# Performance work log

Hardware: AMD Instinct MI355X
Metric: run time of the kernel (lower is better)

The kernel has to match this reference:

```python
import jax, jax.numpy as jnp
import numpy as np

N_NODES = 50000
N_EDGES = 800000
F = 64
R = 32


def setup_inputs() -> dict:
    key = jax.random.key(0)
    ks = jax.random.split(key, 12)
    s = jax.random.normal(ks[0], (N_NODES, F), dtype=jnp.float32)
    v = jax.random.normal(ks[1], (N_NODES, 3, F), dtype=jnp.float32)
    radial_embeddings = jax.random.normal(ks[2], (N_EDGES, R), dtype=jnp.float32)
    f_cut = jax.random.uniform(ks[3], (N_EDGES,), dtype=jnp.float32)
    unit_vectors = jax.random.normal(ks[4], (N_EDGES, 3), dtype=jnp.float32)
    edge_index = jax.random.randint(ks[5], (2, N_EDGES), 0, N_NODES, dtype=jnp.int64 if jax.config.jax_enable_x64 else jnp.int32)
    # mlp_phi: Linear(F,F) -> SiLU -> Linear(F, 3F); linear_W: Linear(R, 3F)
    W1 = jax.random.normal(ks[6], (F, F), dtype=jnp.float32) / np.sqrt(F)
    b1 = jnp.zeros((F,), dtype=jnp.float32)
    W2 = jax.random.normal(ks[7], (F, 3 * F), dtype=jnp.float32) / np.sqrt(F)
    b2 = jnp.zeros((3 * F,), dtype=jnp.float32)
    Wr = jax.random.normal(ks[8], (R, 3 * F), dtype=jnp.float32) / np.sqrt(R)
    br = jnp.zeros((3 * F,), dtype=jnp.float32)
    return {"s": s, "v": v, "radial_embeddings": radial_embeddings, "f_cut": f_cut,
            "unit_vectors": unit_vectors, "edge_index": edge_index,
            "W1": W1, "b1": b1, "W2": W2, "b2": b2, "Wr": Wr, "br": br}


def reference(s, v, radial_embeddings, f_cut, unit_vectors, edge_index, W1, b1, W2, b2, Wr, br):
    idx_i, idx_j = edge_index[0], edge_index[1]
    n_nodes = s.shape[0]
    nf = s.shape[-1]
    # per-node MLP: Linear -> SiLU -> Linear to 3F channels
    phi = jax.nn.silu(s @ W1 + b1) @ W2 + b2            # [N, 3F]
    # radial filter weighted by cutoff
    W = (radial_embeddings @ Wr + br) * f_cut[:, None]   # [E, 3F]
    x = phi[idx_j] * W                                   # [E, 3F]  (gather + multiply)
    x_s, x_vv, x_vs = x[:, :nf], x[:, nf:2 * nf], x[:, 2 * nf:]
    ds = jax.ops.segment_sum(x_s, idx_i, num_segments=n_nodes)          # [N, F]
    x_v = v[idx_j] * x_vv[:, None, :] + x_vs[:, None, :] * unit_vectors[:, :, None]  # [E, 3, F]
    dv = jax.ops.segment_sum(x_v, idx_i, num_segments=n_nodes)          # [N, 3, F]
    return s + ds, v + dv
```

## Files before the change

kernel.cpp:

```cpp
#include <hip/hip_runtime.h>
#include <math.h>

#define N_NODES 50000
#define N_EDGES 800000
#define F 64
#define R 32
#define C3F 192
#define CAP 48
#define MLP_BLOCKS ((N_NODES + 31) / 32)
#define FILL_BLOCKS ((N_EDGES + 255) / 256)

#define REP32(X) X(0) X(1) X(2) X(3) X(4) X(5) X(6) X(7) \
                 X(8) X(9) X(10) X(11) X(12) X(13) X(14) X(15) \
                 X(16) X(17) X(18) X(19) X(20) X(21) X(22) X(23) \
                 X(24) X(25) X(26) X(27) X(28) X(29) X(30) X(31)

__global__ __launch_bounds__(256) void mlp_fill_kernel(
    const float* __restrict__ s, const float* __restrict__ W1,
    const float* __restrict__ b1, const float* __restrict__ W2,
    const float* __restrict__ b2, float* __restrict__ phi,
    const int* __restrict__ eidx, int* __restrict__ counts,
    int2* __restrict__ bucket)
{
    __shared__ float hid_s[32][68];

    if (blockIdx.x >= MLP_BLOCKS) {
        int e = (blockIdx.x - MLP_BLOCKS) * 256 + threadIdx.x;
        if (e < N_EDGES) {
            int i = eidx[e];
            int j = eidx[N_EDGES + e];
            int pos = atomicAdd(&counts[i], 1);
            if (pos < CAP) bucket[(size_t)i * CAP + pos] = make_int2(e, j);
        }
        return;
    }

    int n = threadIdx.x >> 3;
    int seg = threadIdx.x & 7;
    int node = blockIdx.x * 32 + n;
    bool live = node < N_NODES;

    if (live) {
        float sv[F];
        const float4* srow = (const float4*)(s + (size_t)node * F);
#pragma unroll
        for (int q = 0; q < F / 4; q++) {
            float4 t = srow[q];
            sv[4*q+0] = t.x; sv[4*q+1] = t.y; sv[4*q+2] = t.z; sv[4*q+3] = t.w;
        }
        float acc[8];
#pragma unroll
        for (int q = 0; q < 8; q++) acc[q] = b1[seg * 8 + q];
#pragma unroll
        for (int k = 0; k < F; k++) {
            float sk = sv[k];
            const float4* w = (const float4*)(W1 + (size_t)k * F + seg * 8);
            float4 w0 = w[0], w1 = w[1];
            acc[0] += sk * w0.x; acc[1] += sk * w0.y;
            acc[2] += sk * w0.z; acc[3] += sk * w0.w;
            acc[4] += sk * w1.x; acc[5] += sk * w1.y;
            acc[6] += sk * w1.z; acc[7] += sk * w1.w;
        }
#pragma unroll
        for (int q = 0; q < 8; q++) {
            float a = acc[q];
            hid_s[n][seg * 8 + q] = a / (1.f + __expf(-a));
        }
    }
    __syncthreads();

    if (!live) return;

    float hv[F];
#pragma unroll
    for (int q = 0; q < F; q++) hv[q] = hid_s[n][q];

    float acc[24];
#pragma unroll
    for (int q = 0; q < 24; q++) acc[q] = b2[seg * 24 + q];
#pragma unroll
    for (int k = 0; k < F; k++) {
        float hk = hv[k];
        const float4* w = (const float4*)(W2 + (size_t)k * C3F + seg * 24);
#pragma unroll
        for (int q4 = 0; q4 < 6; q4++) {
            float4 wv = w[q4];
            acc[q4*4+0] += hk * wv.x;
            acc[q4*4+1] += hk * wv.y;
            acc[q4*4+2] += hk * wv.z;
            acc[q4*4+3] += hk * wv.w;
        }
    }
    float4* o = (float4*)(phi + (size_t)node * C3F + seg * 24);
#pragma unroll
    for (int q4 = 0; q4 < 6; q4++)
        o[q4] = make_float4(acc[q4*4+0], acc[q4*4+1], acc[q4*4+2], acc[q4*4+3]);
}

__global__ __launch_bounds__(256, 3) void gather_kernel(
    const float* __restrict__ s, const float* __restrict__ v,
    const float* __restrict__ phi, const float* __restrict__ radial,
    const float* __restrict__ f_cut, const float* __restrict__ unit_vec,
    const float* __restrict__ Wr, const float* __restrict__ br,
    const int* __restrict__ counts, const int2* __restrict__ bucket,
    float* __restrict__ out_s, float* __restrict__ out_v)
{
    int lane = threadIdx.x & 63;
    int node = __builtin_amdgcn_readfirstlane(
        (int)blockIdx.x * 4 + (int)(threadIdx.x >> 6));
    if (node >= N_NODES) return;

#define DECL_WR(r) float wrs##r, wrv##r, wrq##r;
    REP32(DECL_WR)
#undef DECL_WR
#define LOAD_WR(r) { const float* w_ = Wr + (r) * C3F; \
                     wrs##r = w_[lane]; wrv##r = w_[64 + lane]; \
                     wrq##r = w_[128 + lane]; }
    REP32(LOAD_WR)
#undef LOAD_WR

    float b_s = br[lane], b_vv = br[64 + lane], b_vs = br[128 + lane];

    float acc_s = 0.f, acc_v0 = 0.f, acc_v1 = 0.f, acc_v2 = 0.f;

    int cnt = __builtin_amdgcn_readfirstlane(counts[node]);
    cnt = cnt < CAP ? cnt : CAP;
    const int2* row = bucket + (size_t)node * CAP;

    if (cnt > 0) {
        int2 ej0 = row[0];
        int e = __builtin_amdgcn_readfirstlane(ej0.x);
        int j = __builtin_amdgcn_readfirstlane(ej0.y);
        const float* pj = phi + (size_t)j * C3F;
        const float* vj = v + (size_t)j * C3F;
        float ps = pj[lane], pvv = pj[64 + lane], pvs = pj[128 + lane];
        float va = vj[lane], vb = vj[64 + lane], vc = vj[128 + lane];

        for (int k = 0; k < cnt; k++) {
            float fc = f_cut[e];
            float u0 = unit_vec[e * 3 + 0];
            float u1 = unit_vec[e * 3 + 1];
            float u2 = unit_vec[e * 3 + 2];
            const float* rp = radial + (size_t)e * R;

            int e_n = e, j_n = j;
            if (k + 1 < cnt) {
                int2 ejn = row[k + 1];
                e_n = __builtin_amdgcn_readfirstlane(ejn.x);
                j_n = __builtin_amdgcn_readfirstlane(ejn.y);
            }
            const float* pn = phi + (size_t)j_n * C3F;
            const float* vn = v + (size_t)j_n * C3F;
            float nps = pn[lane], npvv = pn[64 + lane], npvs = pn[128 + lane];
            float nva = vn[lane], nvb = vn[64 + lane], nvc = vn[128 + lane];

            float ws = b_s, wvv = b_vv, wvs = b_vs;
#define FMA_WR(r) { float rr = rp[r]; ws += rr * wrs##r; \
                    wvv += rr * wrv##r; wvs += rr * wrq##r; }
            REP32(FMA_WR)
#undef FMA_WR

            float xs  = ps  * ws  * fc;
            float xvv = pvv * wvv * fc;
            float xvs = pvs * wvs * fc;
            acc_s  += xs;
            acc_v0 += va * xvv + xvs * u0;
            acc_v1 += vb * xvv + xvs * u1;
            acc_v2 += vc * xvv + xvs * u2;

            e = e_n; j = j_n;
            ps = nps; pvv = npvv; pvs = npvs;
            va = nva; vb = nvb; vc = nvc;
        }
    }

    out_s[(size_t)node * F + lane] = s[(size_t)node * F + lane] + acc_s;
    const float* vi = v + (size_t)node * C3F;
    float* ovi = out_v + (size_t)node * C3F;
    ovi[lane]       = vi[lane]       + acc_v0;
    ovi[64 + lane]  = vi[64 + lane]  + acc_v1;
    ovi[128 + lane] = vi[128 + lane] + acc_v2;
}

extern "C" void kernel_launch(void* const* d_in, const int* in_sizes, int n_in,
                              void* d_out, int out_size, void* d_ws, size_t ws_size,
                              hipStream_t stream)
{
    const float* s      = (const float*)d_in[0];
    const float* v      = (const float*)d_in[1];
    const float* radial = (const float*)d_in[2];
    const float* f_cut  = (const float*)d_in[3];
    const float* unit   = (const float*)d_in[4];
    const int*   eidx   = (const int*)  d_in[5];
    const float* W1     = (const float*)d_in[6];
    const float* b1     = (const float*)d_in[7];
    const float* W2     = (const float*)d_in[8];
    const float* b2     = (const float*)d_in[9];
    const float* Wr     = (const float*)d_in[10];
    const float* br     = (const float*)d_in[11];

    float* out   = (float*)d_out;
    float* out_s = out;
    float* out_v = out + (size_t)N_NODES * F;

    float* phi    = (float*)d_ws;
    int*   counts = (int*)(phi + (size_t)N_NODES * C3F);
    int2*  bucket = (int2*)(counts + N_NODES);

    hipMemsetAsync(counts, 0, N_NODES * sizeof(int), stream);

    mlp_fill_kernel<<<MLP_BLOCKS + FILL_BLOCKS, 256, 0, stream>>>(
        s, W1, b1, W2, b2, phi, eidx, counts, bucket);

    gather_kernel<<<(N_NODES + 3) / 4, 256, 0, stream>>>(
        s, v, phi, radial, f_cut, unit, Wr, br,
        counts, bucket, out_s, out_v);
}
```

Measured before the change: 602.2 us.

## Split gather across three wavefronts per node, one per channel segment

```diff
diff --git a/kernel.cpp b/kernel.cpp
--- a/kernel.cpp
+++ b/kernel.cpp
@@ -97,7 +97,113 @@
         o[q4] = make_float4(acc[q4*4+0], acc[q4*4+1], acc[q4*4+2], acc[q4*4+3]);
 }
 
-__global__ __launch_bounds__(256, 3) void gather_kernel(
+template<int W>
+__device__ __forceinline__ void gather_seg(
+    const float* __restrict__ v, const float* __restrict__ phi,
+    const float* __restrict__ radial, const float* __restrict__ f_cut,
+    const float* __restrict__ unit_vec, const float* __restrict__ Wr,
+    const float* __restrict__ br, const int2* __restrict__ row,
+    int cnt, int lane, float& racc0, float& racc1, float& racc2)
+{
+    constexpr int SEG = W * 64;
+
+#define DECL_WR(r) float wr##r;
+    REP32(DECL_WR)
+#undef DECL_WR
+#define LOAD_WR(r) wr##r = Wr[(r) * C3F + SEG + lane];
+    REP32(LOAD_WR)
+#undef LOAD_WR
+    const float bseg = br[SEG + lane];
+
+    float acc0 = 0.f, acc1 = 0.f, acc2 = 0.f;
+
+    if (cnt > 0) {
+        int2 ej0 = row[0];
+        int e = __builtin_amdgcn_readfirstlane(ej0.x);
+        int j = __builtin_amdgcn_readfirstlane(ej0.y);
+
+        float p = phi[(size_t)j * C3F + SEG + lane];
+        float va = 0.f, vb = 0.f, vc = 0.f;
+        if constexpr (W == 1) {
+            const float* vj = v + (size_t)j * C3F;
+            va = vj[lane]; vb = vj[64 + lane]; vc = vj[128 + lane];
+        }
+        float fc = f_cut[e];
+        float u0 = 0.f, u1 = 0.f, u2 = 0.f;
+        if constexpr (W == 2) {
+            u0 = unit_vec[e * 3 + 0];
+            u1 = unit_vec[e * 3 + 1];
+            u2 = unit_vec[e * 3 + 2];
+        }
+#define DECL_CR(r) float cr##r;
+        REP32(DECL_CR)
+#undef DECL_CR
+        {
+            const float* rp = radial + (size_t)e * R;
+#define LOAD_CR(r) cr##r = rp[r];
+            REP32(LOAD_CR)
+#undef LOAD_CR
+        }
+
+        for (int k = 0; k < cnt; ++k) {
+            int e_n = e, j_n = j;
+            if (k + 1 < cnt) {
+                int2 ejn = row[k + 1];
+                e_n = __builtin_amdgcn_readfirstlane(ejn.x);
+                j_n = __builtin_amdgcn_readfirstlane(ejn.y);
+            }
+            float p_n = phi[(size_t)j_n * C3F + SEG + lane];
+            float nva = 0.f, nvb = 0.f, nvc = 0.f;
+            if constexpr (W == 1) {
+                const float* vn = v + (size_t)j_n * C3F;
+                nva = vn[lane]; nvb = vn[64 + lane]; nvc = vn[128 + lane];
+            }
+            float fc_n = f_cut[e_n];
+            float nu0 = 0.f, nu1 = 0.f, nu2 = 0.f;
+            if constexpr (W == 2) {
+                nu0 = unit_vec[e_n * 3 + 0];
+                nu1 = unit_vec[e_n * 3 + 1];
+                nu2 = unit_vec[e_n * 3 + 2];
+            }
+#define DECL_NR(r) float nr##r;
+            REP32(DECL_NR)
+#undef DECL_NR
+            {
+                const float* rpn = radial + (size_t)e_n * R;
+#define LOAD_NR(r) nr##r = rpn[r];
+                REP32(LOAD_NR)
+#undef LOAD_NR
+            }
+
+            float wsum[4] = { bseg, 0.f, 0.f, 0.f };
+#define FMA_WR(r) wsum[(r) & 3] += cr##r * wr##r;
+            REP32(FMA_WR)
+#undef FMA_WR
+            float ws = (wsum[0] + wsum[1]) + (wsum[2] + wsum[3]);
+
+            float x = p * ws * fc;
+            if constexpr (W == 0) {
+                acc0 += x;
+            } else if constexpr (W == 1) {
+                acc0 += va * x; acc1 += vb * x; acc2 += vc * x;
+            } else {
+                acc0 += x * u0; acc1 += x * u1; acc2 += x * u2;
+            }
+
+            e = e_n; j = j_n;
+            p = p_n; fc = fc_n;
+            if constexpr (W == 1) { va = nva; vb = nvb; vc = nvc; }
+            if constexpr (W == 2) { u0 = nu0; u1 = nu1; u2 = nu2; }
+#define ROT_R(r) cr##r = nr##r;
+            REP32(ROT_R)
+#undef ROT_R
+        }
+    }
+
+    racc0 = acc0; racc1 = acc1; racc2 = acc2;
+}
+
+__global__ __launch_bounds__(192, 6) void gather_kernel(
     const float* __restrict__ s, const float* __restrict__ v,
     const float* __restrict__ phi, const float* __restrict__ radial,
     const float* __restrict__ f_cut, const float* __restrict__ unit_vec,
@@ -105,81 +211,36 @@
     const int* __restrict__ counts, const int2* __restrict__ bucket,
     float* __restrict__ out_s, float* __restrict__ out_v)
 {
-    int lane = threadIdx.x & 63;
-    int node = __builtin_amdgcn_readfirstlane(
-        (int)blockIdx.x * 4 + (int)(threadIdx.x >> 6));
-    if (node >= N_NODES) return;
-
-#define DECL_WR(r) float wrs##r, wrv##r, wrq##r;
-    REP32(DECL_WR)
-#undef DECL_WR
-#define LOAD_WR(r) { const float* w_ = Wr + (r) * C3F; \
-                     wrs##r = w_[lane]; wrv##r = w_[64 + lane]; \
-                     wrq##r = w_[128 + lane]; }
-    REP32(LOAD_WR)
-#undef LOAD_WR
-
-    float b_s = br[lane], b_vv = br[64 + lane], b_vs = br[128 + lane];
-
-    float acc_s = 0.f, acc_v0 = 0.f, acc_v1 = 0.f, acc_v2 = 0.f;
+    const int lane = threadIdx.x & 63;
+    const int w    = threadIdx.x >> 6;
+    const int node = blockIdx.x;
+
+    __shared__ float tmp[3][64];
 
     int cnt = __builtin_amdgcn_readfirstlane(counts[node]);
     cnt = cnt < CAP ? cnt : CAP;
     const int2* row = bucket + (size_t)node * CAP;
 
-    if (cnt > 0) {
-        int2 ej0 = row[0];
-        int e = __builtin_amdgcn_readfirstlane(ej0.x);
-        int j = __builtin_amdgcn_readfirstlane(ej0.y);
-        const float* pj = phi + (size_t)j * C3F;
-        const float* vj = v + (size_t)j * C3F;
-        float ps = pj[lane], pvv = pj[64 + lane], pvs = pj[128 + lane];
-        float va = vj[lane], vb = vj[64 + lane], vc = vj[128 + lane];
-
-        for (int k = 0; k < cnt; k++) {
-            float fc = f_cut[e];
-            float u0 = unit_vec[e * 3 + 0];
-            float u1 = unit_vec[e * 3 + 1];
-            float u2 = unit_vec[e * 3 + 2];
-            const float* rp = radial + (size_t)e * R;
-
-            int e_n = e, j_n = j;
-            if (k + 1 < cnt) {
-                int2 ejn = row[k + 1];
-                e_n = __builtin_amdgcn_readfirstlane(ejn.x);
-                j_n = __builtin_amdgcn_readfirstlane(ejn.y);
-            }
-            const float* pn = phi + (size_t)j_n * C3F;
-            const float* vn = v + (size_t)j_n * C3F;
-            float nps = pn[lane], npvv = pn[64 + lane], npvs = pn[128 + lane];
-            float nva = vn[lane], nvb = vn[64 + lane], nvc = vn[128 + lane];
-
-            float ws = b_s, wvv = b_vv, wvs = b_vs;
-#define FMA_WR(r) { float rr = rp[r]; ws += rr * wrs##r; \
-                    wvv += rr * wrv##r; wvs += rr * wrq##r; }
-            REP32(FMA_WR)
-#undef FMA_WR
-
-            float xs  = ps  * ws  * fc;
-            float xvv = pvv * wvv * fc;
-            float xvs = pvs * wvs * fc;
-            acc_s  += xs;
-            acc_v0 += va * xvv + xvs * u0;
-            acc_v1 += vb * xvv + xvs * u1;
-            acc_v2 += vc * xvv + xvs * u2;
-
-            e = e_n; j = j_n;
-            ps = nps; pvv = npvv; pvs = npvs;
-            va = nva; vb = nvb; vc = nvc;
-        }
-    }
-
-    out_s[(size_t)node * F + lane] = s[(size_t)node * F + lane] + acc_s;
-    const float* vi = v + (size_t)node * C3F;
-    float* ovi = out_v + (size_t)node * C3F;
-    ovi[lane]       = vi[lane]       + acc_v0;
-    ovi[64 + lane]  = vi[64 + lane]  + acc_v1;
-    ovi[128 + lane] = vi[128 + lane] + acc_v2;
+    float a0 = 0.f, a1 = 0.f, a2 = 0.f;
+    if (w == 0)
+        gather_seg<0>(v, phi, radial, f_cut, unit_vec, Wr, br, row, cnt, lane, a0, a1, a2);
+    else if (w == 1)
+        gather_seg<1>(v, phi, radial, f_cut, unit_vec, Wr, br, row, cnt, lane, a0, a1, a2);
+    else
+        gather_seg<2>(v, phi, radial, f_cut, unit_vec, Wr, br, row, cnt, lane, a0, a1, a2);
+
+    if (w == 2) { tmp[0][lane] = a0; tmp[1][lane] = a1; tmp[2][lane] = a2; }
+    __syncthreads();
+
+    if (w == 0) {
+        out_s[(size_t)node * F + lane] = s[(size_t)node * F + lane] + a0;
+    } else if (w == 1) {
+        const float* vi = v + (size_t)node * C3F;
+        float* ovi = out_v + (size_t)node * C3F;
+        ovi[lane]       = vi[lane]       + a0 + tmp[0][lane];
+        ovi[64 + lane]  = vi[64 + lane]  + a1 + tmp[1][lane];
+        ovi[128 + lane] = vi[128 + lane] + a2 + tmp[2][lane];
+    }
 }
 
 extern "C" void kernel_launch(void* const* d_in, const int* in_sizes, int n_in,
@@ -212,7 +273,7 @@
     mlp_fill_kernel<<<MLP_BLOCKS + FILL_BLOCKS, 256, 0, stream>>>(
         s, W1, b1, W2, b2, phi, eidx, counts, bucket);
 
-    gather_kernel<<<(N_NODES + 3) / 4, 256, 0, stream>>>(
+    gather_kernel<<<N_NODES, 192, 0, stream>>>(
         s, v, phi, radial, f_cut, unit, Wr, br,
         counts, bucket, out_s, out_v);
 }
```

Measured after the change: 654.5 us. 1.09x slower.

## Prefetch next edge's radial row and pad atomic counters, one wave per block

Applied to the files above, without the earlier changes.

```diff
diff --git a/kernel.cpp b/kernel.cpp
--- a/kernel.cpp
+++ b/kernel.cpp
@@ -7,6 +7,7 @@
 #define R 32
 #define C3F 192
 #define CAP 48
+#define CSTRIDE 16
 #define MLP_BLOCKS ((N_NODES + 31) / 32)
 #define FILL_BLOCKS ((N_EDGES + 255) / 256)
 
@@ -29,7 +30,7 @@
         if (e < N_EDGES) {
             int i = eidx[e];
             int j = eidx[N_EDGES + e];
-            int pos = atomicAdd(&counts[i], 1);
+            int pos = atomicAdd(&counts[i * CSTRIDE], 1);
             if (pos < CAP) bucket[(size_t)i * CAP + pos] = make_int2(e, j);
         }
         return;
@@ -97,7 +98,7 @@
         o[q4] = make_float4(acc[q4*4+0], acc[q4*4+1], acc[q4*4+2], acc[q4*4+3]);
 }
 
-__global__ __launch_bounds__(256, 3) void gather_kernel(
+__global__ __launch_bounds__(64, 4) void gather_kernel(
     const float* __restrict__ s, const float* __restrict__ v,
     const float* __restrict__ phi, const float* __restrict__ radial,
     const float* __restrict__ f_cut, const float* __restrict__ unit_vec,
@@ -105,10 +106,8 @@
     const int* __restrict__ counts, const int2* __restrict__ bucket,
     float* __restrict__ out_s, float* __restrict__ out_v)
 {
-    int lane = threadIdx.x & 63;
-    int node = __builtin_amdgcn_readfirstlane(
-        (int)blockIdx.x * 4 + (int)(threadIdx.x >> 6));
-    if (node >= N_NODES) return;
+    const int lane = threadIdx.x;
+    const int node = blockIdx.x;
 
 #define DECL_WR(r) float wrs##r, wrv##r, wrq##r;
     REP32(DECL_WR)
@@ -118,12 +117,18 @@
                      wrq##r = w_[128 + lane]; }
     REP32(LOAD_WR)
 #undef LOAD_WR
-
-    float b_s = br[lane], b_vv = br[64 + lane], b_vs = br[128 + lane];
+#define KA3(r) , "+v"(wrs##r), "+v"(wrv##r), "+v"(wrq##r)
+    asm volatile("" : "+v"(wrs0) KA3(1) KA3(2) KA3(3) KA3(4) KA3(5) KA3(6) KA3(7), "+v"(wrv0), "+v"(wrq0));
+    asm volatile("" : "+v"(wrs8) KA3(9) KA3(10) KA3(11) KA3(12) KA3(13) KA3(14) KA3(15), "+v"(wrv8), "+v"(wrq8));
+    asm volatile("" : "+v"(wrs16) KA3(17) KA3(18) KA3(19) KA3(20) KA3(21) KA3(22) KA3(23), "+v"(wrv16), "+v"(wrq16));
+    asm volatile("" : "+v"(wrs24) KA3(25) KA3(26) KA3(27) KA3(28) KA3(29) KA3(30) KA3(31), "+v"(wrv24), "+v"(wrq24));
+#undef KA3
+
+    const float b_s = br[lane], b_vv = br[64 + lane], b_vs = br[128 + lane];
 
     float acc_s = 0.f, acc_v0 = 0.f, acc_v1 = 0.f, acc_v2 = 0.f;
 
-    int cnt = __builtin_amdgcn_readfirstlane(counts[node]);
+    int cnt = __builtin_amdgcn_readfirstlane(counts[node * CSTRIDE]);
     cnt = cnt < CAP ? cnt : CAP;
     const int2* row = bucket + (size_t)node * CAP;
 
@@ -131,18 +136,27 @@
         int2 ej0 = row[0];
         int e = __builtin_amdgcn_readfirstlane(ej0.x);
         int j = __builtin_amdgcn_readfirstlane(ej0.y);
+
         const float* pj = phi + (size_t)j * C3F;
         const float* vj = v + (size_t)j * C3F;
         float ps = pj[lane], pvv = pj[64 + lane], pvs = pj[128 + lane];
         float va = vj[lane], vb = vj[64 + lane], vc = vj[128 + lane];
 
-        for (int k = 0; k < cnt; k++) {
-            float fc = f_cut[e];
-            float u0 = unit_vec[e * 3 + 0];
-            float u1 = unit_vec[e * 3 + 1];
-            float u2 = unit_vec[e * 3 + 2];
+        float fc = f_cut[e];
+        float u0 = unit_vec[e * 3 + 0];
+        float u1 = unit_vec[e * 3 + 1];
+        float u2 = unit_vec[e * 3 + 2];
+#define DECL_CR(r) float cr##r;
+        REP32(DECL_CR)
+#undef DECL_CR
+        {
             const float* rp = radial + (size_t)e * R;
-
+#define LOAD_CR(r) cr##r = rp[r];
+            REP32(LOAD_CR)
+#undef LOAD_CR
+        }
+
+        for (int k = 0; k < cnt; ++k) {
             int e_n = e, j_n = j;
             if (k + 1 < cnt) {
                 int2 ejn = row[k + 1];
@@ -153,10 +167,24 @@
             const float* vn = v + (size_t)j_n * C3F;
             float nps = pn[lane], npvv = pn[64 + lane], npvs = pn[128 + lane];
             float nva = vn[lane], nvb = vn[64 + lane], nvc = vn[128 + lane];
+            float fc_n = f_cut[e_n];
+            float nu0 = unit_vec[e_n * 3 + 0];
+            float nu1 = unit_vec[e_n * 3 + 1];
+            float nu2 = unit_vec[e_n * 3 + 2];
+#define DECL_NR(r) float nr##r;
+            REP32(DECL_NR)
+#undef DECL_NR
+            {
+                const float* rpn = radial + (size_t)e_n * R;
+#define LOAD_NR(r) nr##r = rpn[r];
+                REP32(LOAD_NR)
+#undef LOAD_NR
+            }
 
             float ws = b_s, wvv = b_vv, wvs = b_vs;
-#define FMA_WR(r) { float rr = rp[r]; ws += rr * wrs##r; \
-                    wvv += rr * wrv##r; wvs += rr * wrq##r; }
+#define FMA_WR(r) { ws  += cr##r * wrs##r; \
+                    wvv += cr##r * wrv##r; \
+                    wvs += cr##r * wrq##r; }
             REP32(FMA_WR)
 #undef FMA_WR
 
@@ -171,6 +199,10 @@
             e = e_n; j = j_n;
             ps = nps; pvv = npvv; pvs = npvs;
             va = nva; vb = nvb; vc = nvc;
+            fc = fc_n; u0 = nu0; u1 = nu1; u2 = nu2;
+#define ROT_R(r) cr##r = nr##r;
+            REP32(ROT_R)
+#undef ROT_R
         }
     }
 
@@ -205,14 +237,14 @@
 
     float* phi    = (float*)d_ws;
     int*   counts = (int*)(phi + (size_t)N_NODES * C3F);
-    int2*  bucket = (int2*)(counts + N_NODES);
-
-    hipMemsetAsync(counts, 0, N_NODES * sizeof(int), stream);
+    int2*  bucket = (int2*)(counts + (size_t)N_NODES * CSTRIDE);
+
+    hipMemsetAsync(counts, 0, (size_t)N_NODES * CSTRIDE * sizeof(int), stream);
 
     mlp_fill_kernel<<<MLP_BLOCKS + FILL_BLOCKS, 256, 0, stream>>>(
         s, W1, b1, W2, b2, phi, eidx, counts, bucket);
 
-    gather_kernel<<<(N_NODES + 3) / 4, 256, 0, stream>>>(
+    gather_kernel<<<N_NODES, 64, 0, stream>>>(
         s, v, phi, radial, f_cut, unit, Wr, br,
         counts, bucket, out_s, out_v);
 }
```

After: 572.3 us. 1.05x faster.
